# Kernel tuning notes

Measured on AMD Instinct MI355X. Metric: run time of the kernel, lower is better.

The kernel has to match this reference:

```python
import jax, jax.numpy as jnp
import numpy as np

# dims matching init_kwargs
U, T, S, K = 2048, 200, 10, 20   # users, history_length, slate_size, num_topics
DE, DU, V, H = 32, 32, 100000, 16  # doc_embed_dim, user_embed_dim, num_docs, rnn hidden
D_IN = DE + (S + 1) + (S + 1) * K + 1  # 264 concatenated feature width
LEAKY_ALPHA = 0.3  # keras LeakyReLU default


def setup_inputs() -> dict:
    key = jax.random.key(0)
    ks = jax.random.split(key, 9)
    slate_doc_quality_history = jax.random.normal(ks[0], (U, T, S), jnp.float32)
    slate_doc_features_history = jax.random.normal(ks[1], (U, T, S, K), jnp.float32)
    docid_history = jax.random.randint(ks[2], (U, T), 0, V + 1)  # 0 is the masked id
    ctime_history = jax.random.uniform(ks[3], (U, T), jnp.float32)
    # learned parameters
    emb_table = jax.random.normal(ks[4], (V + 1, DE), jnp.float32) * 0.05
    Wx = jax.random.normal(ks[5], (D_IN, H), jnp.float32) * (1.0 / np.sqrt(D_IN))
    Wh = jax.random.normal(ks[6], (H, H), jnp.float32) * (1.0 / np.sqrt(H))
    b_rnn = jnp.zeros((H,), jnp.float32)
    Wd = jax.random.normal(ks[7], (H, DU), jnp.float32) * (1.0 / np.sqrt(H))
    b_dense = jnp.zeros((DU,), jnp.float32)
    return dict(
        slate_doc_quality_history=slate_doc_quality_history,
        slate_doc_features_history=slate_doc_features_history,
        docid_history=docid_history,
        ctime_history=ctime_history,
        emb_table=emb_table, Wx=Wx, Wh=Wh, b_rnn=b_rnn, Wd=Wd, b_dense=b_dense,
    )


def reference(slate_doc_quality_history, slate_doc_features_history, docid_history,
              ctime_history, emb_table, Wx, Wh, b_rnn, Wd, b_dense):
    B, Tlen = docid_history.shape
    # embedding lookup; mask_zero=True -> timesteps with id==0 are skipped by the RNN
    emb = emb_table[docid_history]                                   # [U,T,DE]
    mask = docid_history != 0                                        # [U,T]
    # append zero quality column -> [U,T,S+1]
    q = jnp.concatenate([slate_doc_quality_history,
                         jnp.zeros((B, Tlen, 1), slate_doc_quality_history.dtype)], axis=-1)
    # append zero feature row on slate axis, flatten -> [U,T,(S+1)*K]
    f = jnp.concatenate([slate_doc_features_history,
                         jnp.zeros((B, Tlen, 1, K), slate_doc_features_history.dtype)], axis=-2)
    f = f.reshape(B, Tlen, -1)
    x = jnp.concatenate([emb, q, f, ctime_history[..., None]], axis=-1)  # [U,T,D_IN]

    # SimpleRNN(16): h_t = tanh(x_t Wx + h_{t-1} Wh + b); masked steps keep previous h
    pre = jnp.einsum('btd,dh->bth', x, Wx) + b_rnn                   # [U,T,H]

    def step(h, inp):
        pre_t, m_t = inp                                             # [U,H], [U]
        h_new = jnp.tanh(pre_t + h @ Wh)
        h = jnp.where(m_t[:, None], h_new, h)
        return h, None

    h0 = jnp.zeros((B, Wh.shape[0]), x.dtype)
    hT, _ = jax.lax.scan(step, h0, (pre.transpose(1, 0, 2), mask.T))
    # LeakyReLU(alpha=0.3) then Dense -> user embeddings [U, DU]
    a = jnp.where(hT >= 0, hT, LEAKY_ALPHA * hT)
    return a @ Wd + b_dense
```

## Files before the change

### kernel.cpp

```cpp
#include <hip/hip_runtime.h>

#define U_   2048
#define T_   200
#define S_   10
#define K_   20
#define H_   16
#define DU_  32
#define DE_  32
#define DIN_ 264

__global__ __launch_bounds__(256) void k_pre(
    const float* __restrict__ q, const float* __restrict__ f,
    const int* __restrict__ docid, const float* __restrict__ ct,
    const float* __restrict__ emb, const float* __restrict__ Wx,
    const float* __restrict__ brnn, float* __restrict__ pre)
{
    const int idx = blockIdx.x * 256 + threadIdx.x;

    float acc[H_];
#pragma unroll
    for (int h = 0; h < H_; ++h) acc[h] = brnn[h];

    {
        const float4* f4 = (const float4*)(f + (size_t)idx * (S_ * K_));
#pragma unroll 5
        for (int r = 0; r < (S_ * K_) / 4; ++r) {
            float4 v = f4[r];
            const float* w = Wx + (DE_ + S_ + 1 + r * 4) * H_;
#pragma unroll
            for (int h = 0; h < H_; ++h)
                acc[h] += v.x * w[h] + v.y * w[h + 16] + v.z * w[h + 32] + v.w * w[h + 48];
        }
    }

    {
        const float4* e4 = (const float4*)(emb + (size_t)docid[idx] * DE_);
#pragma unroll
        for (int r = 0; r < DE_ / 4; ++r) {
            float4 v = e4[r];
            const float* w = Wx + (r * 4) * H_;
#pragma unroll
            for (int h = 0; h < H_; ++h)
                acc[h] += v.x * w[h] + v.y * w[h + 16] + v.z * w[h + 32] + v.w * w[h + 48];
        }
    }

    {
        const float2* q2 = (const float2*)(q + (size_t)idx * S_);
#pragma unroll
        for (int r = 0; r < S_ / 2; ++r) {
            float2 v = q2[r];
            const float* w = Wx + (DE_ + r * 2) * H_;
#pragma unroll
            for (int h = 0; h < H_; ++h)
                acc[h] += v.x * w[h] + v.y * w[h + 16];
        }
    }

    {
        float c = ct[idx];
        const float* w = Wx + (DIN_ - 1) * H_;
#pragma unroll
        for (int h = 0; h < H_; ++h) acc[h] += c * w[h];
    }

    float4* o = (float4*)(pre + (size_t)idx * H_);
    o[0] = make_float4(acc[0], acc[1], acc[2], acc[3]);
    o[1] = make_float4(acc[4], acc[5], acc[6], acc[7]);
    o[2] = make_float4(acc[8], acc[9], acc[10], acc[11]);
    o[3] = make_float4(acc[12], acc[13], acc[14], acc[15]);
}

__device__ __forceinline__ float tanh_fast(float x) {
    float e = __expf(2.f * x);
    return 1.f - 2.f / (e + 1.f);
}

__global__ __launch_bounds__(64) void k_rnn(
    const float* __restrict__ pre, const int* __restrict__ docid,
    const float* __restrict__ Wh, const float* __restrict__ Wd,
    const float* __restrict__ bd, float* __restrict__ out)
{
    const int tid = threadIdx.x;
    const int l = tid & 15;
    const int u = (blockIdx.x * 64 + tid) >> 4;

    const float* prow = pre + (size_t)u * T_ * H_;
    const int* drow = docid + (size_t)u * T_;

    float wh[16];
#pragma unroll
    for (int k = 0; k < 16; ++k) wh[k] = Wh[((l ^ k) << 4) | l];

    float h = 0.f;

    float pb0 = prow[0 * H_ + l], pb1 = prow[1 * H_ + l],
          pb2 = prow[2 * H_ + l], pb3 = prow[3 * H_ + l];
    int   m0 = drow[0], m1 = drow[1], m2 = drow[2], m3 = drow[3];

    for (int tb = 0; tb < T_; tb += 4) {
#pragma unroll
        for (int s = 0; s < 4; ++s) {
            float p; int m;
            if      (s == 0) { p = pb0; m = m0; }
            else if (s == 1) { p = pb1; m = m1; }
            else if (s == 2) { p = pb2; m = m2; }
            else             { p = pb3; m = m3; }

            int tn = tb + 4 + s; if (tn > T_ - 1) tn = T_ - 1;
            float pn = prow[tn * H_ + l];
            int   mn = drow[tn];
            if      (s == 0) { pb0 = pn; m0 = mn; }
            else if (s == 1) { pb1 = pn; m1 = mn; }
            else if (s == 2) { pb2 = pn; m2 = mn; }
            else             { pb3 = pn; m3 = mn; }

            float a0 = p, a1 = 0.f, a2 = 0.f, a3 = 0.f;
#pragma unroll
            for (int k = 0; k < 16; k += 4) {
                a0 += __shfl_xor(h, k + 0, 16) * wh[k + 0];
                a1 += __shfl_xor(h, k + 1, 16) * wh[k + 1];
                a2 += __shfl_xor(h, k + 2, 16) * wh[k + 2];
                a3 += __shfl_xor(h, k + 3, 16) * wh[k + 3];
            }
            float accv = (a0 + a1) + (a2 + a3);
            float th = tanh_fast(accv);
            h = (m != 0) ? th : h;
        }
    }

    float a = (h >= 0.f) ? h : 0.3f * h;

    float wd0[16], wd1[16];
#pragma unroll
    for (int k = 0; k < 16; ++k) {
        int j = l ^ k;
        wd0[k] = Wd[j * DU_ + l];
        wd1[k] = Wd[j * DU_ + l + 16];
    }
    float o0 = bd[l], o1 = bd[l + 16];
#pragma unroll
    for (int k = 0; k < 16; ++k) {
        float av = __shfl_xor(a, k, 16);
        o0 += av * wd0[k];
        o1 += av * wd1[k];
    }
    out[(size_t)u * DU_ + l] = o0;
    out[(size_t)u * DU_ + l + 16] = o1;
}

extern "C" void kernel_launch(void* const* d_in, const int* in_sizes, int n_in,
                              void* d_out, int out_size, void* d_ws, size_t ws_size,
                              hipStream_t stream) {
    const float* q     = (const float*)d_in[0];
    const float* f     = (const float*)d_in[1];
    const int*   docid = (const int*)  d_in[2];
    const float* ct    = (const float*)d_in[3];
    const float* emb   = (const float*)d_in[4];
    const float* Wx    = (const float*)d_in[5];
    const float* Wh    = (const float*)d_in[6];
    const float* brnn  = (const float*)d_in[7];
    const float* Wd    = (const float*)d_in[8];
    const float* bd    = (const float*)d_in[9];
    float* out = (float*)d_out;

    float* pre = (float*)d_ws;

    k_pre<<<(U_ * T_) / 256, 256, 0, stream>>>(q, f, docid, ct, emb, Wx, brnn, pre);
    k_rnn<<<(U_ * H_) / 64, 64, 0, stream>>>(pre, docid, Wh, Wd, bd, out);
}
```

Before: 175.2 us.

## Compute feature projection with split-bf16 MFMA and separate embedding kernel

The 200-wide slate-feature part of the input projection moves to MFMA 16x16x32 bf16 instructions. Both operands are split into hi/lo bf16 halves and three products are accumulated to keep close to fp32 accuracy, with a small prep kernel that transposes and splits Wx. The embedding, quality and ctime terms go to a separate scalar kernel that reads the partial result back and adds to it. The aim is to cut the FP32 FMA cost of the dominant matmul, at the price of an extra kernel launch and an extra read-modify-write pass over the pre buffer.

```diff
diff --git a/kernel.cpp b/kernel.cpp
--- a/kernel.cpp
+++ b/kernel.cpp
@@ -9,66 +9,174 @@
 #define DE_  32
 #define DIN_ 264
 
-__global__ __launch_bounds__(256) void k_pre(
-    const float* __restrict__ q, const float* __restrict__ f,
-    const int* __restrict__ docid, const float* __restrict__ ct,
-    const float* __restrict__ emb, const float* __restrict__ Wx,
-    const float* __restrict__ brnn, float* __restrict__ pre)
+#define KPAD 224
+
+typedef __attribute__((ext_vector_type(8))) short bf16x8;
+typedef __attribute__((ext_vector_type(4))) float f32x4;
+
+__device__ __forceinline__ unsigned short bf16_rne(float x) {
+    unsigned u = __float_as_uint(x);
+    return (unsigned short)((u + 0x7FFFu + ((u >> 16) & 1u)) >> 16);
+}
+
+__global__ __launch_bounds__(256) void k_wprep(
+    const float* __restrict__ Wx,
+    unsigned short* __restrict__ WThi, unsigned short* __restrict__ WTlo)
 {
     const int idx = blockIdx.x * 256 + threadIdx.x;
+    if (idx >= 16 * KPAD) return;
+    const int n = idx / KPAD, k = idx - n * KPAD;
+    const float wv = (k < 200) ? Wx[(43 + k) * H_ + n] : 0.f;
+    const unsigned short h = bf16_rne(wv);
+    const float hf = __uint_as_float((unsigned)h << 16);
+    WThi[idx] = h;
+    WTlo[idx] = bf16_rne(wv - hf);
+}
+
+__global__ __launch_bounds__(256, 4) void k_pre_f(
+    const float* __restrict__ f,
+    const unsigned short* __restrict__ WThi,
+    const unsigned short* __restrict__ WTlo,
+    float* __restrict__ pre)
+{
+    __shared__ unsigned short lds_hi[4][64][32];
+    __shared__ unsigned short lds_lo[4][64][32];
+    const int t = threadIdx.x;
+    const int l = t & 63;
+    const int w = t >> 6;
+    const int rbase = blockIdx.x * 256 + w * 64;
+    const char* fB = (const char*)f;
+
+    f32x4 acc[4];
+#pragma unroll
+    for (int fi = 0; fi < 4; ++fi) acc[fi] = (f32x4){0.f, 0.f, 0.f, 0.f};
+
+    auto LOADF = [&](float4* dst, int s) {
+        if (s < 6) {
+#pragma unroll
+            for (int i = 0; i < 8; ++i) {
+                const int row = rbase + i * 8 + (l >> 3);
+                dst[i] = *(const float4*)(fB + (size_t)row * 800 + s * 128 + (l & 7) * 16);
+            }
+        } else {
+#pragma unroll
+            for (int i = 0; i < 2; ++i) {
+                const int row = rbase + i * 32 + (l >> 1);
+                dst[i] = *(const float4*)(fB + (size_t)row * 800 + 768 + (l & 1) * 16);
+            }
+        }
+    };
+
+    auto WR4 = [&](int pos, int kq, float4 v) {
+        const unsigned short h0 = bf16_rne(v.x), h1 = bf16_rne(v.y),
+                             h2 = bf16_rne(v.z), h3 = bf16_rne(v.w);
+        const float r0 = v.x - __uint_as_float((unsigned)h0 << 16);
+        const float r1 = v.y - __uint_as_float((unsigned)h1 << 16);
+        const float r2 = v.z - __uint_as_float((unsigned)h2 << 16);
+        const float r3 = v.w - __uint_as_float((unsigned)h3 << 16);
+        uint2 hv, lv;
+        hv.x = (unsigned)h0 | ((unsigned)h1 << 16);
+        hv.y = (unsigned)h2 | ((unsigned)h3 << 16);
+        lv.x = (unsigned)bf16_rne(r0) | ((unsigned)bf16_rne(r1) << 16);
+        lv.y = (unsigned)bf16_rne(r2) | ((unsigned)bf16_rne(r3) << 16);
+        *(uint2*)&lds_hi[w][pos][kq] = hv;
+        *(uint2*)&lds_lo[w][pos][kq] = lv;
+    };
+
+    auto CVTW = [&](const float4* src, int s) {
+        if (s < 6) {
+#pragma unroll
+            for (int i = 0; i < 8; ++i)
+                WR4(i * 8 + (l >> 3), (l & 7) * 4, src[i]);
+        } else {
+#pragma unroll
+            for (int i = 0; i < 2; ++i)
+                WR4(i * 32 + (l >> 1), (l & 1) * 4, src[i]);
+        }
+    };
+
+    float4 bufA[8], bufB[8];
+    LOADF(bufA, 0);
+
+#pragma unroll
+    for (int s = 0; s < 7; ++s) {
+        const float4* cur = (s & 1) ? bufB : bufA;
+        float4* nxt = (s & 1) ? bufA : bufB;
+        if (s < 6) LOADF(nxt, s + 1);
+
+        CVTW(cur, s);
+
+        const bf16x8 bh = *(const bf16x8*)(WThi + (l & 15) * KPAD + s * 32 + (l >> 4) * 8);
+        const bf16x8 bl = *(const bf16x8*)(WTlo + (l & 15) * KPAD + s * 32 + (l >> 4) * 8);
+
+#pragma unroll
+        for (int fi = 0; fi < 4; ++fi) {
+            const int pl_ = fi * 16 + (l & 15);
+            const bf16x8 ah = *(const bf16x8*)&lds_hi[w][pl_][(l >> 4) * 8];
+            const bf16x8 al = *(const bf16x8*)&lds_lo[w][pl_][(l >> 4) * 8];
+            acc[fi] = __builtin_amdgcn_mfma_f32_16x16x32_bf16(ah, bh, acc[fi], 0, 0, 0);
+            acc[fi] = __builtin_amdgcn_mfma_f32_16x16x32_bf16(al, bh, acc[fi], 0, 0, 0);
+            acc[fi] = __builtin_amdgcn_mfma_f32_16x16x32_bf16(ah, bl, acc[fi], 0, 0, 0);
+        }
+    }
+
+#pragma unroll
+    for (int fi = 0; fi < 4; ++fi) {
+#pragma unroll
+        for (int r = 0; r < 4; ++r) {
+            const int pos = rbase + fi * 16 + (l >> 4) * 4 + r;
+            pre[(size_t)pos * H_ + (l & 15)] = acc[fi][r];
+        }
+    }
+}
+
+__global__ __launch_bounds__(256) void k_emb(
+    const float* __restrict__ q, const int* __restrict__ docid,
+    const float* __restrict__ ct, const float* __restrict__ emb,
+    const float* __restrict__ Wx, const float* __restrict__ brnn,
+    float* __restrict__ pre)
+{
+    const int idx = blockIdx.x * 256 + threadIdx.x;
 
     float acc[H_];
 #pragma unroll
     for (int h = 0; h < H_; ++h) acc[h] = brnn[h];
-
-    {
-        const float4* f4 = (const float4*)(f + (size_t)idx * (S_ * K_));
-#pragma unroll 5
-        for (int r = 0; r < (S_ * K_) / 4; ++r) {
-            float4 v = f4[r];
-            const float* w = Wx + (DE_ + S_ + 1 + r * 4) * H_;
-#pragma unroll
-            for (int h = 0; h < H_; ++h)
-                acc[h] += v.x * w[h] + v.y * w[h + 16] + v.z * w[h + 32] + v.w * w[h + 48];
-        }
-    }
 
     {
         const float4* e4 = (const float4*)(emb + (size_t)docid[idx] * DE_);
 #pragma unroll
         for (int r = 0; r < DE_ / 4; ++r) {
-            float4 v = e4[r];
-            const float* w = Wx + (r * 4) * H_;
+            const float4 v = e4[r];
+            const float* wt = Wx + (r * 4) * H_;
 #pragma unroll
             for (int h = 0; h < H_; ++h)
-                acc[h] += v.x * w[h] + v.y * w[h + 16] + v.z * w[h + 32] + v.w * w[h + 48];
-        }
-    }
-
+                acc[h] += v.x * wt[h] + v.y * wt[h + 16] + v.z * wt[h + 32] + v.w * wt[h + 48];
+        }
+    }
     {
         const float2* q2 = (const float2*)(q + (size_t)idx * S_);
 #pragma unroll
         for (int r = 0; r < S_ / 2; ++r) {
-            float2 v = q2[r];
-            const float* w = Wx + (DE_ + r * 2) * H_;
+            const float2 v = q2[r];
+            const float* wt = Wx + (DE_ + 2 * r) * H_;
 #pragma unroll
             for (int h = 0; h < H_; ++h)
-                acc[h] += v.x * w[h] + v.y * w[h + 16];
-        }
-    }
-
+                acc[h] += v.x * wt[h] + v.y * wt[h + 16];
+        }
+    }
     {
-        float c = ct[idx];
-        const float* w = Wx + (DIN_ - 1) * H_;
-#pragma unroll
-        for (int h = 0; h < H_; ++h) acc[h] += c * w[h];
+        const float c = ct[idx];
+        const float* wt = Wx + (DIN_ - 1) * H_;
+#pragma unroll
+        for (int h = 0; h < H_; ++h) acc[h] += c * wt[h];
     }
 
     float4* o = (float4*)(pre + (size_t)idx * H_);
-    o[0] = make_float4(acc[0], acc[1], acc[2], acc[3]);
-    o[1] = make_float4(acc[4], acc[5], acc[6], acc[7]);
-    o[2] = make_float4(acc[8], acc[9], acc[10], acc[11]);
-    o[3] = make_float4(acc[12], acc[13], acc[14], acc[15]);
+    float4 p0 = o[0], p1 = o[1], p2 = o[2], p3 = o[3];
+    o[0] = make_float4(p0.x + acc[0],  p0.y + acc[1],  p0.z + acc[2],  p0.w + acc[3]);
+    o[1] = make_float4(p1.x + acc[4],  p1.y + acc[5],  p1.z + acc[6],  p1.w + acc[7]);
+    o[2] = make_float4(p2.x + acc[8],  p2.y + acc[9],  p2.z + acc[10], p2.w + acc[11]);
+    o[3] = make_float4(p3.x + acc[12], p3.y + acc[13], p3.z + acc[14], p3.w + acc[15]);
 }
 
 __device__ __forceinline__ float tanh_fast(float x) {
@@ -165,7 +273,11 @@
     float* out = (float*)d_out;
 
     float* pre = (float*)d_ws;
-
-    k_pre<<<(U_ * T_) / 256, 256, 0, stream>>>(q, f, docid, ct, emb, Wx, brnn, pre);
+    unsigned short* WThi = (unsigned short*)((char*)d_ws + (size_t)U_ * T_ * H_ * 4);
+    unsigned short* WTlo = WThi + 16 * KPAD;
+
+    k_wprep<<<(16 * KPAD + 255) / 256, 256, 0, stream>>>(Wx, WThi, WTlo);
+    k_pre_f<<<(U_ * T_) / 256, 256, 0, stream>>>(f, WThi, WTlo, pre);
+    k_emb<<<(U_ * T_) / 256, 256, 0, stream>>>(q, docid, ct, emb, Wx, brnn, pre);
     k_rnn<<<(U_ * H_) / 64, 64, 0, stream>>>(pre, docid, Wh, Wd, bd, out);
 }
```

New measurement: 174.5 us. No clear change (-0.4%).

## Compute input projection with split-bf16 MFMA and LDS-staged feature tiles

Applied to the files above, without the earlier changes.

Replaces the per-thread scalar FMA projection of the 264-wide features onto 16 hidden units with MFMA 16x16x32 bf16 instructions. Each wave handles 16 rows. Feature rows are loaded coalesced into a padded LDS pane. Precision is kept near fp32 by splitting both operands into hi and lo bf16 parts and summing three products. A small prep kernel transposes, pads and splits Wx each call, adding one extra launch and a small loss of precision from dropping the lo-lo term.

```diff
diff --git a/kernel.cpp b/kernel.cpp
--- a/kernel.cpp
+++ b/kernel.cpp
@@ -2,73 +2,141 @@
 
 #define U_   2048
 #define T_   200
-#define S_   10
-#define K_   20
 #define H_   16
 #define DU_  32
-#define DE_  32
-#define DIN_ 264
-
-__global__ __launch_bounds__(256) void k_pre(
-    const float* __restrict__ q, const float* __restrict__ f,
+#define KP   288
+
+typedef __attribute__((ext_vector_type(8))) short bf16x8;
+typedef __attribute__((ext_vector_type(4))) float f32x4;
+
+__device__ __forceinline__ unsigned short bf16_rne(float x) {
+    unsigned u = __float_as_uint(x);
+    return (unsigned short)((u + 0x7FFFu + ((u >> 16) & 1u)) >> 16);
+}
+
+__device__ __forceinline__ void cvt8(const float* x, bf16x8& hi, bf16x8& lo) {
+    union { bf16x8 v; unsigned u[4]; } H, L;
+#pragma unroll
+    for (int i = 0; i < 4; ++i) {
+        const unsigned short h0 = bf16_rne(x[2 * i]), h1 = bf16_rne(x[2 * i + 1]);
+        const float r0 = x[2 * i]     - __uint_as_float((unsigned)h0 << 16);
+        const float r1 = x[2 * i + 1] - __uint_as_float((unsigned)h1 << 16);
+        H.u[i] = (unsigned)h0 | ((unsigned)h1 << 16);
+        L.u[i] = (unsigned)bf16_rne(r0) | ((unsigned)bf16_rne(r1) << 16);
+    }
+    hi = H.v; lo = L.v;
+}
+
+__global__ __launch_bounds__(256) void k_wprep(
+    const float* __restrict__ Wx,
+    unsigned short* __restrict__ WThi, unsigned short* __restrict__ WTlo)
+{
+    const int idx = blockIdx.x * 256 + threadIdx.x;
+    if (idx >= 16 * KP) return;
+    const int n = idx / KP, k = idx - n * KP;
+    const int s = k >> 5, kk = k & 31;
+    float wv = 0.f;
+    if (s < 7)       { if (k < 200) wv = Wx[(43 + k) * H_ + n]; }
+    else if (s == 7) { wv = Wx[kk * H_ + n]; }
+    else             { if (kk < 10) wv = Wx[(32 + kk) * H_ + n];
+                       else if (kk == 10) wv = Wx[263 * H_ + n]; }
+    const unsigned short h = bf16_rne(wv);
+    WThi[idx] = h;
+    WTlo[idx] = bf16_rne(wv - __uint_as_float((unsigned)h << 16));
+}
+
+__global__ __launch_bounds__(256, 3) void k_pre(
+    const float* __restrict__ qh, const float* __restrict__ f,
     const int* __restrict__ docid, const float* __restrict__ ct,
-    const float* __restrict__ emb, const float* __restrict__ Wx,
+    const float* __restrict__ emb,
+    const unsigned short* __restrict__ WThi,
+    const unsigned short* __restrict__ WTlo,
     const float* __restrict__ brnn, float* __restrict__ pre)
 {
-    const int idx = blockIdx.x * 256 + threadIdx.x;
-
-    float acc[H_];
-#pragma unroll
-    for (int h = 0; h < H_; ++h) acc[h] = brnn[h];
+    __shared__ float pane[4][16 * 204];
+    const int t = threadIdx.x, l = t & 63, w = t >> 6;
+    const int tile = blockIdx.x * 4 + w;
+    const int rbase = tile * 16;
+    const int r = l & 15, qd = l >> 4;
+    const int pos = rbase + r;
+
+    const char* fsrc = (const char*)f + (size_t)rbase * 800;
+    float4 buf[13];
+#pragma unroll
+    for (int m = 0; m < 13; ++m)
+        if (m < 12 || l < 32)
+            buf[m] = *(const float4*)(fsrc + (size_t)(m * 64 + l) * 16);
+
+    const int did = docid[pos];
+    const float4 e0 = *(const float4*)(emb + (size_t)did * 32 + qd * 8);
+    const float4 e1 = *(const float4*)(emb + (size_t)did * 32 + qd * 8 + 4);
+
+    float qx[8];
+#pragma unroll
+    for (int i = 0; i < 8; ++i) qx[i] = 0.f;
+    if (qd == 0) {
+#pragma unroll
+        for (int j = 0; j < 4; ++j) {
+            float2 v = *(const float2*)(qh + (size_t)pos * 10 + 2 * j);
+            qx[2 * j] = v.x; qx[2 * j + 1] = v.y;
+        }
+    } else if (qd == 1) {
+        qx[0] = qh[(size_t)pos * 10 + 8];
+        qx[1] = qh[(size_t)pos * 10 + 9];
+        qx[2] = ct[pos];
+    }
+    const float bias = brnn[r];
+
+    float* pn = pane[w];
+#pragma unroll
+    for (int m = 0; m < 13; ++m) {
+        const int g = m * 64 + l;
+        if (g < 800) *(float4*)(pn + 4 * (g + g / 50)) = buf[m];
+    }
+
+    f32x4 acc = {bias, bias, bias, bias};
+
+#pragma unroll
+    for (int s = 0; s < 7; ++s) {
+        float xr[8];
+        if (s < 6 || qd == 0) {
+            const float4 a0 = *(const float4*)(pn + r * 204 + s * 32 + qd * 8);
+            const float4 a1 = *(const float4*)(pn + r * 204 + s * 32 + qd * 8 + 4);
+            xr[0] = a0.x; xr[1] = a0.y; xr[2] = a0.z; xr[3] = a0.w;
+            xr[4] = a1.x; xr[5] = a1.y; xr[6] = a1.z; xr[7] = a1.w;
+        } else {
+#pragma unroll
+            for (int i = 0; i < 8; ++i) xr[i] = 0.f;
+        }
+        bf16x8 ah, al; cvt8(xr, ah, al);
+        const bf16x8 bh = *(const bf16x8*)(WThi + r * KP + s * 32 + qd * 8);
+        const bf16x8 bl = *(const bf16x8*)(WTlo + r * KP + s * 32 + qd * 8);
+        acc = __builtin_amdgcn_mfma_f32_16x16x32_bf16(ah, bh, acc, 0, 0, 0);
+        acc = __builtin_amdgcn_mfma_f32_16x16x32_bf16(al, bh, acc, 0, 0, 0);
+        acc = __builtin_amdgcn_mfma_f32_16x16x32_bf16(ah, bl, acc, 0, 0, 0);
+    }
 
     {
-        const float4* f4 = (const float4*)(f + (size_t)idx * (S_ * K_));
-#pragma unroll 5
-        for (int r = 0; r < (S_ * K_) / 4; ++r) {
-            float4 v = f4[r];
-            const float* w = Wx + (DE_ + S_ + 1 + r * 4) * H_;
-#pragma unroll
-            for (int h = 0; h < H_; ++h)
-                acc[h] += v.x * w[h] + v.y * w[h + 16] + v.z * w[h + 32] + v.w * w[h + 48];
-        }
-    }
-
+        float xr[8] = {e0.x, e0.y, e0.z, e0.w, e1.x, e1.y, e1.z, e1.w};
+        bf16x8 ah, al; cvt8(xr, ah, al);
+        const bf16x8 bh = *(const bf16x8*)(WThi + r * KP + 7 * 32 + qd * 8);
+        const bf16x8 bl = *(const bf16x8*)(WTlo + r * KP + 7 * 32 + qd * 8);
+        acc = __builtin_amdgcn_mfma_f32_16x16x32_bf16(ah, bh, acc, 0, 0, 0);
+        acc = __builtin_amdgcn_mfma_f32_16x16x32_bf16(al, bh, acc, 0, 0, 0);
+        acc = __builtin_amdgcn_mfma_f32_16x16x32_bf16(ah, bl, acc, 0, 0, 0);
+    }
     {
-        const float4* e4 = (const float4*)(emb + (size_t)docid[idx] * DE_);
-#pragma unroll
-        for (int r = 0; r < DE_ / 4; ++r) {
-            float4 v = e4[r];
-            const float* w = Wx + (r * 4) * H_;
-#pragma unroll
-            for (int h = 0; h < H_; ++h)
-                acc[h] += v.x * w[h] + v.y * w[h + 16] + v.z * w[h + 32] + v.w * w[h + 48];
-        }
-    }
-
-    {
-        const float2* q2 = (const float2*)(q + (size_t)idx * S_);
-#pragma unroll
-        for (int r = 0; r < S_ / 2; ++r) {
-            float2 v = q2[r];
-            const float* w = Wx + (DE_ + r * 2) * H_;
-#pragma unroll
-            for (int h = 0; h < H_; ++h)
-                acc[h] += v.x * w[h] + v.y * w[h + 16];
-        }
-    }
-
-    {
-        float c = ct[idx];
-        const float* w = Wx + (DIN_ - 1) * H_;
-#pragma unroll
-        for (int h = 0; h < H_; ++h) acc[h] += c * w[h];
-    }
-
-    float4* o = (float4*)(pre + (size_t)idx * H_);
-    o[0] = make_float4(acc[0], acc[1], acc[2], acc[3]);
-    o[1] = make_float4(acc[4], acc[5], acc[6], acc[7]);
-    o[2] = make_float4(acc[8], acc[9], acc[10], acc[11]);
-    o[3] = make_float4(acc[12], acc[13], acc[14], acc[15]);
+        bf16x8 ah, al; cvt8(qx, ah, al);
+        const bf16x8 bh = *(const bf16x8*)(WThi + r * KP + 8 * 32 + qd * 8);
+        const bf16x8 bl = *(const bf16x8*)(WTlo + r * KP + 8 * 32 + qd * 8);
+        acc = __builtin_amdgcn_mfma_f32_16x16x32_bf16(ah, bh, acc, 0, 0, 0);
+        acc = __builtin_amdgcn_mfma_f32_16x16x32_bf16(al, bh, acc, 0, 0, 0);
+        acc = __builtin_amdgcn_mfma_f32_16x16x32_bf16(ah, bl, acc, 0, 0, 0);
+    }
+
+#pragma unroll
+    for (int i = 0; i < 4; ++i)
+        pre[(size_t)(rbase + qd * 4 + i) * H_ + r] = acc[i];
 }
 
 __device__ __forceinline__ float tanh_fast(float x) {
@@ -152,7 +220,7 @@
 extern "C" void kernel_launch(void* const* d_in, const int* in_sizes, int n_in,
                               void* d_out, int out_size, void* d_ws, size_t ws_size,
                               hipStream_t stream) {
-    const float* q     = (const float*)d_in[0];
+    const float* qh    = (const float*)d_in[0];
     const float* f     = (const float*)d_in[1];
     const int*   docid = (const int*)  d_in[2];
     const float* ct    = (const float*)d_in[3];
@@ -165,7 +233,10 @@
     float* out = (float*)d_out;
 
     float* pre = (float*)d_ws;
-
-    k_pre<<<(U_ * T_) / 256, 256, 0, stream>>>(q, f, docid, ct, emb, Wx, brnn, pre);
+    unsigned short* WThi = (unsigned short*)((char*)d_ws + (size_t)U_ * T_ * H_ * 4);
+    unsigned short* WTlo = WThi + 16 * KP;
+
+    k_wprep<<<(16 * KP + 255) / 256, 256, 0, stream>>>(Wx, WThi, WTlo);
+    k_pre<<<(U_ * T_) / 64, 256, 0, stream>>>(qh, f, docid, ct, emb, WThi, WTlo, brnn, pre);
     k_rnn<<<(U_ * H_) / 64, 64, 0, stream>>>(pre, docid, Wh, Wd, bd, out);
 }
```

Result: faster. 153.2 us (median of 2 runs) (-12.6%).
